# Kernel optimization log

Hardware: AMD Instinct MI355X
Metric: run time of the kernel (lower is better)

The kernel has to match this reference:

```python
import jax, jax.numpy as jnp
import numpy as np

IN_FEATURES = 2048
OUT_FEATURES = 2048
BATCH = 32768
EPS = 1e-10

def setup_inputs() -> dict:
    key = jax.random.key(0)
    kx, kp = jax.random.split(key)
    x = jax.random.normal(kx, (BATCH, IN_FEATURES), dtype=jnp.float32)
    P = jax.random.normal(kp, (OUT_FEATURES, IN_FEATURES), dtype=jnp.float32)
    bias = jnp.zeros((OUT_FEATURES,), dtype=jnp.float32)
    return {"x": x, "P": P, "bias": bias}

def reference(x, P, bias):
    # Gram matrix of columns of P: [in, in]
    PTP = jnp.abs(P.T @ P)
    # per-column (dim=0 sum) AOL rescaling factor: [in]
    d = 1.0 / jnp.sqrt(PTP.sum(axis=0) + EPS)
    # W = P @ diag(d) == column-wise scale of P
    W = P * d[None, :]          # [out, in]
    return x @ W.T + bias        # [batch, out]
```

## Files before the change

### kernel.cpp

```cpp
#include <hip/hip_runtime.h>
#include <hip/hip_bf16.h>
#include <stdint.h>

#define IN_F  2048
#define OUT_F 2048
#define BATCH 32768

typedef __attribute__((ext_vector_type(8))) short  short8;
typedef __attribute__((ext_vector_type(4))) float  floatx4;

static constexpr int LDT = 40;

__device__ __forceinline__ uint16_t f2bf(float f) {
  union { float f; uint32_t u; } v; v.f = f;
  uint32_t r = v.u + 0x7FFFu + ((v.u >> 16) & 1u);
  return (uint16_t)(r >> 16);
}

__device__ __forceinline__ void gemm128_pipeline(
    const uint16_t* __restrict__ A, const uint16_t* __restrict__ B,
    int bm, int bn, int K, uint16_t* sA, uint16_t* sB,
    floatx4 (&acc)[4][4]) {
  const int tid  = threadIdx.x;
  const int wave = tid >> 6, lane = tid & 63;
  const int wm = (wave >> 1) * 64, wn = (wave & 1) * 64;

  const int srow = wave * 32 + (lane >> 2);
  const int scol = (lane & 3) * 8;
  const uint16_t* gA = A + (size_t)(bm + srow) * K + scol;
  const uint16_t* gB = B + (size_t)(bn + srow) * K + scol;

  const int wAo  = srow * LDT + scol;
  const int wAo2 = (srow + 16) * LDT + scol;

  const int ra = (wm + (lane & 15)) * LDT + (lane >> 4) * 8;
  const int rb = (wn + (lane & 15)) * LDT + (lane >> 4) * 8;

  short8 rA0 = *(const short8*)gA;
  short8 rA1 = *(const short8*)(gA + 16 * (size_t)K);
  short8 rB0 = *(const short8*)gB;
  short8 rB1 = *(const short8*)(gB + 16 * (size_t)K);
  gA += 32; gB += 32;
  *(short8*)&sA[wAo]  = rA0;  *(short8*)&sA[wAo2] = rA1;
  *(short8*)&sB[wAo]  = rB0;  *(short8*)&sB[wAo2] = rB1;
  __syncthreads();

  const int NK = K / 32;
  int p = 0;
  for (int k = 0; k < NK; k++, p ^= 1) {
    if (k + 1 < NK) {
      rA0 = *(const short8*)gA;
      rA1 = *(const short8*)(gA + 16 * (size_t)K);
      rB0 = *(const short8*)gB;
      rB1 = *(const short8*)(gB + 16 * (size_t)K);
      gA += 32; gB += 32;
    }
    const uint16_t* cA = sA + p * (128 * LDT);
    const uint16_t* cB = sB + p * (128 * LDT);
    short8 af[4], bf[4];
#pragma unroll
    for (int i = 0; i < 4; i++) {
      af[i] = *(const short8*)&cA[ra + i * 16 * LDT];
      bf[i] = *(const short8*)&cB[rb + i * 16 * LDT];
    }
#pragma unroll
    for (int i = 0; i < 4; i++)
#pragma unroll
      for (int j = 0; j < 4; j++)
        acc[i][j] = __builtin_amdgcn_mfma_f32_16x16x32_bf16(af[i], bf[j], acc[i][j], 0, 0, 0);
    if (k + 1 < NK) {
      uint16_t* dA = sA + (p ^ 1) * (128 * LDT);
      uint16_t* dB = sB + (p ^ 1) * (128 * LDT);
      *(short8*)&dA[wAo]  = rA0;  *(short8*)&dA[wAo2] = rA1;
      *(short8*)&dB[wAo]  = rB0;  *(short8*)&dB[wAo2] = rB1;
    }
    __syncthreads();
  }
}

__global__ __launch_bounds__(256) void k_prep(
    const float* __restrict__ P, uint16_t* __restrict__ PT,
    uint16_t* __restrict__ PB) {
  __shared__ float tile[32][33];
  const int bx = blockIdx.x * 32;
  const int by = blockIdx.y * 32;
  const int tx = threadIdx.x & 31;
  const int ty = threadIdx.x >> 5;
#pragma unroll
  for (int i = 0; i < 32; i += 8) {
    float v = P[(size_t)(by + ty + i) * IN_F + bx + tx];
    tile[ty + i][tx] = v;
    PB[(size_t)(by + ty + i) * IN_F + bx + tx] = f2bf(v);
  }
  __syncthreads();
#pragma unroll
  for (int i = 0; i < 32; i += 8)
    PT[(size_t)(bx + ty + i) * IN_F + by + tx] = f2bf(tile[tx][ty + i]);
}

__global__ __launch_bounds__(256) void k_gram_colsum(
    const uint16_t* __restrict__ PT, float* __restrict__ colsum) {
  __shared__ __align__(16) uint16_t sA[2 * 128 * LDT];
  __shared__ __align__(16) uint16_t sB[2 * 128 * LDT];
  __shared__ float colpart[128];

  const int tid = threadIdx.x;
  const int wave = tid >> 6, lane = tid & 63;
  const int bm = blockIdx.x * 128, bn = blockIdx.y * 128;
  const int wn = (wave & 1) * 64;

  floatx4 z = {0.f, 0.f, 0.f, 0.f};
  floatx4 acc[4][4];
#pragma unroll
  for (int i = 0; i < 4; i++)
#pragma unroll
    for (int j = 0; j < 4; j++) acc[i][j] = z;

  gemm128_pipeline(PT, PT, bm, bn, OUT_F, sA, sB, acc);

  if (tid < 128) colpart[tid] = 0.f;
  __syncthreads();
#pragma unroll
  for (int j = 0; j < 4; j++) {
    float s = 0.f;
#pragma unroll
    for (int i = 0; i < 4; i++)
#pragma unroll
      for (int r = 0; r < 4; r++) s += fabsf(acc[i][j][r]);
    atomicAdd(&colpart[wn + j * 16 + (lane & 15)], s);
  }
  __syncthreads();
  if (tid < 128) atomicAdd(&colsum[bn + tid], colpart[tid]);
}

__global__ void k_finalize_d(const float* __restrict__ colsum, float* __restrict__ dv) {
  int i = blockIdx.x * blockDim.x + threadIdx.x;
  if (i < IN_F) dv[i] = 1.0f / sqrtf(colsum[i] + 1e-10f);
}

__global__ __launch_bounds__(256) void k_cvt_x(
    const float4* __restrict__ X4, const float4* __restrict__ dv4,
    uint4* __restrict__ XB) {
  size_t t = (size_t)blockIdx.x * 256 + threadIdx.x;
  int c4 = (int)((2 * t) & (IN_F / 4 - 1));
  float4 a = X4[2 * t], b = X4[2 * t + 1];
  float4 d0 = dv4[c4], d1 = dv4[c4 + 1];
  uint4 o;
  o.x = (uint32_t)f2bf(a.x * d0.x) | ((uint32_t)f2bf(a.y * d0.y) << 16);
  o.y = (uint32_t)f2bf(a.z * d0.z) | ((uint32_t)f2bf(a.w * d0.w) << 16);
  o.z = (uint32_t)f2bf(b.x * d1.x) | ((uint32_t)f2bf(b.y * d1.y) << 16);
  o.w = (uint32_t)f2bf(b.z * d1.z) | ((uint32_t)f2bf(b.w * d1.w) << 16);
  XB[t] = o;
}

__global__ __launch_bounds__(256) void k_gemm_nt(
    const uint16_t* __restrict__ A,
    const uint16_t* __restrict__ B,
    const float* __restrict__ bias,
    float* __restrict__ C) {
  __shared__ __align__(16) uint16_t sA[2 * 128 * LDT];
  __shared__ __align__(16) uint16_t sB[2 * 128 * LDT];

  const int tid = threadIdx.x;
  const int wave = tid >> 6, lane = tid & 63;
  const int bm = blockIdx.x * 128;
  const int bn = blockIdx.y * 128;
  const int wm = (wave >> 1) * 64, wn = (wave & 1) * 64;

  floatx4 z = {0.f, 0.f, 0.f, 0.f};
  floatx4 acc[4][4];
#pragma unroll
  for (int i = 0; i < 4; i++)
#pragma unroll
    for (int j = 0; j < 4; j++) acc[i][j] = z;

  gemm128_pipeline(A, B, bm, bn, IN_F, sA, sB, acc);

#pragma unroll
  for (int j = 0; j < 4; j++) {
    const int col = bn + wn + j * 16 + (lane & 15);
    const float bv = bias[col];
#pragma unroll
    for (int i = 0; i < 4; i++) {
      const int row0 = bm + wm + i * 16 + (lane >> 4) * 4;
#pragma unroll
      for (int r = 0; r < 4; r++)
        C[(size_t)(row0 + r) * OUT_F + col] = acc[i][j][r] + bv;
    }
  }
}

__global__ __launch_bounds__(256) void fb_gram(const float* __restrict__ P,
                                               float* __restrict__ colsum) {
  __shared__ float red[256];
  const int j = blockIdx.x;
  float s = 0.f;
  for (int i = threadIdx.x; i < IN_F; i += 256) {
    float dot = 0.f;
    for (int k = 0; k < OUT_F; k++)
      dot = fmaf(P[(size_t)k * IN_F + i], P[(size_t)k * IN_F + j], dot);
    s += fabsf(dot);
  }
  red[threadIdx.x] = s;
  __syncthreads();
  for (int st = 128; st > 0; st >>= 1) {
    if (threadIdx.x < st) red[threadIdx.x] += red[threadIdx.x + st];
    __syncthreads();
  }
  if (threadIdx.x == 0) colsum[j] = red[0];
}

__global__ __launch_bounds__(256) void fb_gemm(
    const float* __restrict__ X, const float* __restrict__ P,
    const float* __restrict__ dv, const float* __restrict__ bias,
    float* __restrict__ out) {
  __shared__ __align__(16) float xs[64][20];
  __shared__ __align__(16) float ps[64][20];
  const int bm = blockIdx.x * 64, bn = blockIdx.y * 64;
  const int tx = threadIdx.x & 15, ty = threadIdx.x >> 4;
  float acc[4][4] = {};
  const int r = threadIdx.x >> 2, kc = (threadIdx.x & 3) * 4;
  for (int k0 = 0; k0 < IN_F; k0 += 16) {
    float4 xv = *(const float4*)&X[(size_t)(bm + r) * IN_F + k0 + kc];
    float4 pv = *(const float4*)&P[(size_t)(bn + r) * IN_F + k0 + kc];
    float4 dd = *(const float4*)&dv[k0 + kc];
    float4 pw; pw.x = pv.x * dd.x; pw.y = pv.y * dd.y; pw.z = pv.z * dd.z; pw.w = pv.w * dd.w;
    *(float4*)&xs[r][kc] = xv;
    *(float4*)&ps[r][kc] = pw;
    __syncthreads();
#pragma unroll
    for (int kk = 0; kk < 16; kk++) {
      float a0[4], b0[4];
#pragma unroll
      for (int i = 0; i < 4; i++) a0[i] = xs[ty * 4 + i][kk];
#pragma unroll
      for (int jj = 0; jj < 4; jj++) b0[jj] = ps[tx * 4 + jj][kk];
#pragma unroll
      for (int i = 0; i < 4; i++)
#pragma unroll
        for (int jj = 0; jj < 4; jj++) acc[i][jj] = fmaf(a0[i], b0[jj], acc[i][jj]);
    }
    __syncthreads();
  }
#pragma unroll
  for (int i = 0; i < 4; i++)
#pragma unroll
    for (int jj = 0; jj < 4; jj++) {
      int row = bm + ty * 4 + i, col = bn + tx * 4 + jj;
      out[(size_t)row * OUT_F + col] = acc[i][jj] + bias[col];
    }
}

extern "C" void kernel_launch(void* const* d_in, const int* in_sizes, int n_in,
                              void* d_out, int out_size, void* d_ws, size_t ws_size,
                              hipStream_t stream) {
  const float* x    = (const float*)d_in[0];
  const float* P    = (const float*)d_in[1];
  const float* bias = (const float*)d_in[2];
  float* out = (float*)d_out;
  char* ws = (char*)d_ws;

  const size_t SZ_PT = (size_t)IN_F * OUT_F * 2;
  const size_t SZ_PB = (size_t)IN_F * OUT_F * 2;
  const size_t SZ_XB = (size_t)BATCH * IN_F * 2;
  const size_t need  = SZ_PT + SZ_PB + SZ_XB + 2 * IN_F * sizeof(float) + 256;

  if (ws_size >= need) {
    uint16_t* PT = (uint16_t*)ws;
    uint16_t* PB = (uint16_t*)(ws + SZ_PT);
    uint16_t* XB = (uint16_t*)(ws + SZ_PT + SZ_PB);
    float* colsum = (float*)(ws + SZ_PT + SZ_PB + SZ_XB);
    float* dv = colsum + IN_F;

    hipMemsetAsync(colsum, 0, IN_F * sizeof(float), stream);
    k_prep<<<dim3(64, 64), 256, 0, stream>>>(P, PT, PB);
    k_gram_colsum<<<dim3(16, 16), 256, 0, stream>>>(PT, colsum);
    k_finalize_d<<<8, 256, 0, stream>>>(colsum, dv);
    k_cvt_x<<<(int)(((size_t)BATCH * IN_F / 8) / 256), 256, 0, stream>>>(
        (const float4*)x, (const float4*)dv, (uint4*)XB);
    k_gemm_nt<<<dim3(BATCH / 128, OUT_F / 128), 256, 0, stream>>>(XB, PB, bias, out);
  } else {
    float* colsum = (float*)ws;
    float* dv = colsum + IN_F;
    fb_gram<<<IN_F, 256, 0, stream>>>(P, colsum);
    k_finalize_d<<<8, 256, 0, stream>>>(colsum, dv);
    fb_gemm<<<dim3(BATCH / 64, OUT_F / 64), 256, 0, stream>>>(x, P, dv, bias, out);
  }
}
```

Measured before the change: 882.8 us.

## Load GEMM tiles directly to LDS and swap grid order for reuse

Replaces register-staged global loads plus LDS stores with direct global-to-LDS loads (global_load_lds, 16 bytes), which removes the VGPR staging and the separate LDS write step in the shared GEMM pipeline. Because the direct load writes lanes contiguously, the LDS row pitch drops from 40 to 32 and the padding is lost, which risks bank conflicts on the MFMA fragment reads. The main GEMM grid is also transposed so consecutive blocks share the same X row tile across output-column tiles, which should improve L2 reuse of the large activation matrix.

```diff
diff --git a/kernel.cpp b/kernel.cpp
--- a/kernel.cpp
+++ b/kernel.cpp
@@ -9,12 +9,19 @@
 typedef __attribute__((ext_vector_type(8))) short  short8;
 typedef __attribute__((ext_vector_type(4))) float  floatx4;
 
-static constexpr int LDT = 40;
+static constexpr int LDT = 32;
+static constexpr int TILE_USH = 128 * LDT;
 
 __device__ __forceinline__ uint16_t f2bf(float f) {
   union { float f; uint32_t u; } v; v.f = f;
   uint32_t r = v.u + 0x7FFFu + ((v.u >> 16) & 1u);
   return (uint16_t)(r >> 16);
+}
+
+__device__ __forceinline__ void gl_lds16(const uint16_t* g, uint16_t* l) {
+  __builtin_amdgcn_global_load_lds(
+      (const __attribute__((address_space(1))) unsigned int*)(g),
+      (__attribute__((address_space(3))) unsigned int*)(l), 16, 0, 0);
 }
 
 __device__ __forceinline__ void gemm128_pipeline(
@@ -25,38 +32,38 @@
   const int wave = tid >> 6, lane = tid & 63;
   const int wm = (wave >> 1) * 64, wn = (wave & 1) * 64;
 
-  const int srow = wave * 32 + (lane >> 2);
+  const int r0   = wave * 32 + (lane >> 2);
   const int scol = (lane & 3) * 8;
-  const uint16_t* gA = A + (size_t)(bm + srow) * K + scol;
-  const uint16_t* gB = B + (size_t)(bn + srow) * K + scol;
-
-  const int wAo  = srow * LDT + scol;
-  const int wAo2 = (srow + 16) * LDT + scol;
+  const uint16_t* gA = A + (size_t)(bm + r0) * K + scol;
+  const uint16_t* gB = B + (size_t)(bn + r0) * K + scol;
+  const size_t rowK16 = (size_t)16 * K;
+
+  const int ch0 = wave * 2 * (16 * LDT);
+  const int ch1 = ch0 + 16 * LDT;
 
   const int ra = (wm + (lane & 15)) * LDT + (lane >> 4) * 8;
   const int rb = (wn + (lane & 15)) * LDT + (lane >> 4) * 8;
 
-  short8 rA0 = *(const short8*)gA;
-  short8 rA1 = *(const short8*)(gA + 16 * (size_t)K);
-  short8 rB0 = *(const short8*)gB;
-  short8 rB1 = *(const short8*)(gB + 16 * (size_t)K);
+  gl_lds16(gA,          sA + ch0);
+  gl_lds16(gA + rowK16, sA + ch1);
+  gl_lds16(gB,          sB + ch0);
+  gl_lds16(gB + rowK16, sB + ch1);
   gA += 32; gB += 32;
-  *(short8*)&sA[wAo]  = rA0;  *(short8*)&sA[wAo2] = rA1;
-  *(short8*)&sB[wAo]  = rB0;  *(short8*)&sB[wAo2] = rB1;
   __syncthreads();
 
   const int NK = K / 32;
   int p = 0;
   for (int k = 0; k < NK; k++, p ^= 1) {
     if (k + 1 < NK) {
-      rA0 = *(const short8*)gA;
-      rA1 = *(const short8*)(gA + 16 * (size_t)K);
-      rB0 = *(const short8*)gB;
-      rB1 = *(const short8*)(gB + 16 * (size_t)K);
+      const int q = (p ^ 1) * TILE_USH;
+      gl_lds16(gA,          sA + q + ch0);
+      gl_lds16(gA + rowK16, sA + q + ch1);
+      gl_lds16(gB,          sB + q + ch0);
+      gl_lds16(gB + rowK16, sB + q + ch1);
       gA += 32; gB += 32;
     }
-    const uint16_t* cA = sA + p * (128 * LDT);
-    const uint16_t* cB = sB + p * (128 * LDT);
+    const uint16_t* cA = sA + p * TILE_USH;
+    const uint16_t* cB = sB + p * TILE_USH;
     short8 af[4], bf[4];
 #pragma unroll
     for (int i = 0; i < 4; i++) {
@@ -68,12 +75,6 @@
 #pragma unroll
       for (int j = 0; j < 4; j++)
         acc[i][j] = __builtin_amdgcn_mfma_f32_16x16x32_bf16(af[i], bf[j], acc[i][j], 0, 0, 0);
-    if (k + 1 < NK) {
-      uint16_t* dA = sA + (p ^ 1) * (128 * LDT);
-      uint16_t* dB = sB + (p ^ 1) * (128 * LDT);
-      *(short8*)&dA[wAo]  = rA0;  *(short8*)&dA[wAo2] = rA1;
-      *(short8*)&dB[wAo]  = rB0;  *(short8*)&dB[wAo2] = rB1;
-    }
     __syncthreads();
   }
 }
@@ -100,8 +101,8 @@
 
 __global__ __launch_bounds__(256) void k_gram_colsum(
     const uint16_t* __restrict__ PT, float* __restrict__ colsum) {
-  __shared__ __align__(16) uint16_t sA[2 * 128 * LDT];
-  __shared__ __align__(16) uint16_t sB[2 * 128 * LDT];
+  __shared__ __align__(16) uint16_t sA[2 * TILE_USH];
+  __shared__ __align__(16) uint16_t sB[2 * TILE_USH];
   __shared__ float colpart[128];
 
   const int tid = threadIdx.x;
@@ -158,13 +159,13 @@
     const uint16_t* __restrict__ B,
     const float* __restrict__ bias,
     float* __restrict__ C) {
-  __shared__ __align__(16) uint16_t sA[2 * 128 * LDT];
-  __shared__ __align__(16) uint16_t sB[2 * 128 * LDT];
+  __shared__ __align__(16) uint16_t sA[2 * TILE_USH];
+  __shared__ __align__(16) uint16_t sB[2 * TILE_USH];
 
   const int tid = threadIdx.x;
   const int wave = tid >> 6, lane = tid & 63;
-  const int bm = blockIdx.x * 128;
-  const int bn = blockIdx.y * 128;
+  const int bm = blockIdx.y * 128;
+  const int bn = blockIdx.x * 128;
   const int wm = (wave >> 1) * 64, wn = (wave & 1) * 64;
 
   floatx4 z = {0.f, 0.f, 0.f, 0.f};
@@ -278,7 +279,7 @@
     k_finalize_d<<<8, 256, 0, stream>>>(colsum, dv);
     k_cvt_x<<<(int)(((size_t)BATCH * IN_F / 8) / 256), 256, 0, stream>>>(
         (const float4*)x, (const float4*)dv, (uint4*)XB);
-    k_gemm_nt<<<dim3(BATCH / 128, OUT_F / 128), 256, 0, stream>>>(XB, PB, bias, out);
+    k_gemm_nt<<<dim3(OUT_F / 128, BATCH / 128), 256, 0, stream>>>(XB, PB, bias, out);
   } else {
     float* colsum = (float*)ws;
     float* dv = colsum + IN_F;
```

Measured after the change: 833.8 us. 5.6% less time.
